# Performance work log

Measured on AMD Instinct MI355X. Metric: run time of the kernel, lower is better.

Reference implementation:

```python
import jax, jax.numpy as jnp
import numpy as np

B, S, D, H, NI, NB = 512, 200, 256, 4, 100000, 2
DH = D // H
NEG = float(-(2**32) + 1)
SCALE = float(1.0 / np.sqrt(DH))


def ln(x, g, b, eps=1e-3):
    # keras LayerNormalization (default epsilon=1e-3)
    m = jnp.mean(x, axis=-1, keepdims=True)
    v = jnp.var(x, axis=-1, keepdims=True)
    return (x - m) * jax.lax.rsqrt(v + eps) * g + b


def setup_inputs() -> dict:
    key = jax.random.key(0)
    ks = jax.random.split(key, 10)
    s = 0.02
    return {
        "input_ids": jax.random.randint(ks[0], (B, S), 0, NI + 1, dtype=jnp.int32),
        "item_emb": jax.random.normal(ks[1], (NI + 1, D), jnp.float32) * s,
        "pos_emb": jax.random.normal(ks[2], (S, D), jnp.float32) * s,
        "ln1_g": jnp.ones((NB, D), jnp.float32),
        "ln1_b": jnp.zeros((NB, D), jnp.float32),
        "wq": jax.random.normal(ks[3], (NB, D, D), jnp.float32) * s,
        "bq": jnp.zeros((NB, D), jnp.float32),
        "wk": jax.random.normal(ks[4], (NB, D, D), jnp.float32) * s,
        "bk": jnp.zeros((NB, D), jnp.float32),
        "wv": jax.random.normal(ks[5], (NB, D, D), jnp.float32) * s,
        "bv": jnp.zeros((NB, D), jnp.float32),
        "ln2_g": jnp.ones((NB, D), jnp.float32),
        "ln2_b": jnp.zeros((NB, D), jnp.float32),
        "wd": jax.random.normal(ks[6], (NB, D, D), jnp.float32) * s,
        "bd": jnp.zeros((NB, D), jnp.float32),
        "seq_g": jnp.ones((D,), jnp.float32),
        "seq_b": jnp.zeros((D,), jnp.float32),
        "out_item_emb": jax.random.normal(ks[7], (NI, D), jnp.float32) * s,
    }


def reference(input_ids, item_emb, pos_emb, ln1_g, ln1_b, wq, bq, wk, bk, wv, bv,
              ln2_g, ln2_b, wd, bd, seq_g, seq_b, out_item_emb):
    seq = item_emb[input_ids] + pos_emb[None]                      # [B,S,D]
    mask = (input_ids != NI).astype(seq.dtype)[:, :, None]        # pad id == num_items
    causal = jnp.tril(jnp.ones((S, S), bool))
    for i in range(NB):
        x = ln(seq, ln1_g[i], ln1_b[i])                            # queries (pre-norm)
        q = (x @ wq[i] + bq[i]).reshape(B, S, H, DH).transpose(0, 2, 1, 3)
        k = (seq @ wk[i] + bk[i]).reshape(B, S, H, DH).transpose(0, 2, 1, 3)
        v = (seq @ wv[i] + bv[i]).reshape(B, S, H, DH).transpose(0, 2, 1, 3)
        scores = jnp.einsum('bhqd,bhkd->bhqk', q, k) * SCALE       # [B,H,S,S]
        scores = jnp.where(causal, scores, NEG)
        attn = jax.nn.softmax(scores, axis=-1)
        o = jnp.einsum('bhqk,bhkd->bhqd', attn, v)
        o = o.transpose(0, 2, 1, 3).reshape(B, S, D)
        x2 = o + x                                                 # residual to normed queries
        y = jax.nn.relu(ln(x2, ln2_g[i], ln2_b[i]) @ wd[i] + bd[i])
        seq = (y + x2) * mask
    seq_emb = ln(seq[:, -1, :], seq_g, seq_b)                      # [B,D]
    return seq_emb @ out_item_emb.T                                # [B,num_items], linear act
```

## Files before the change

### kernel.cpp

```cpp
#include <hip/hip_runtime.h>
#include <hip/hip_bf16.h>
#include <cstdint>
#include <cstddef>

namespace {
constexpr int B = 512, S = 200, D = 256, H = 4, DH = 64, NI = 100000;
constexpr float EPS = 1e-3f;
constexpr float SCALE = 0.125f;
}

typedef __attribute__((ext_vector_type(8))) short bf16x8;
typedef __attribute__((ext_vector_type(4))) float f32x4;

__device__ inline unsigned short f2b(float f) {
  union { float f; unsigned int u; } v; v.f = f;
  unsigned int r = v.u + 0x7FFFu + ((v.u >> 16) & 1u);
  return (unsigned short)(r >> 16);
}

__device__ inline float b2f(unsigned short u) {
  union { unsigned int i; float f; } x; x.i = (unsigned int)u << 16; return x.f;
}

__device__ inline bf16x8 pack8(float4 a, float4 b) {
  bf16x8 r;
  r[0] = (short)f2b(a.x); r[1] = (short)f2b(a.y); r[2] = (short)f2b(a.z); r[3] = (short)f2b(a.w);
  r[4] = (short)f2b(b.x); r[5] = (short)f2b(b.y); r[6] = (short)f2b(b.z); r[7] = (short)f2b(b.w);
  return r;
}

__device__ inline ushort4 pack4(float4 a) {
  ushort4 r;
  r.x = f2b(a.x); r.y = f2b(a.y); r.z = f2b(a.z); r.w = f2b(a.w);
  return r;
}

__device__ inline float4 unpack4(ushort4 u) {
  float4 r; r.x = b2f(u.x); r.y = b2f(u.y); r.z = b2f(u.z); r.w = b2f(u.w); return r;
}

__device__ inline void gload_lds16(const unsigned short* g, unsigned short* l) {
  __builtin_amdgcn_global_load_lds((const __attribute__((address_space(1))) void*)g,
                                   (__attribute__((address_space(3))) void*)l, 16, 0, 0);
}

__global__ void cvt_wt_k(const float* __restrict__ wq, const float* __restrict__ wk,
                         const float* __restrict__ wv, const float* __restrict__ wd,
                         unsigned short* __restrict__ dst) {
  const int t = blockIdx.x * 256 + threadIdx.x;
  const int w = t >> 14, rem = t & 16383;
  const int k = rem >> 6, n4 = (rem & 63) * 4;
  const int blk = w >> 2, which = w & 3;
  const float* src = (which == 0 ? wq : which == 1 ? wk : which == 2 ? wv : wd) + blk * 65536;
  const float4 v = *(const float4*)(src + k * 256 + n4);
  unsigned short* d = dst + w * 65536;
  d[(n4 + 0) * 256 + k] = f2b(v.x);
  d[(n4 + 1) * 256 + k] = f2b(v.y);
  d[(n4 + 2) * 256 + k] = f2b(v.z);
  d[(n4 + 3) * 256 + k] = f2b(v.w);
}

__global__ __launch_bounds__(256) void embed_ln_k(const int* __restrict__ ids,
                                                  const float* __restrict__ ie,
                                                  const float* __restrict__ pe,
                                                  const float* __restrict__ g1,
                                                  const float* __restrict__ b1,
                                                  unsigned short* __restrict__ seq_bf,
                                                  unsigned short* __restrict__ x_bf) {
  const int row = blockIdx.x * 4 + (threadIdx.x >> 6);
  const int lane = threadIdx.x & 63;
  const int id = ids[row];
  const int s = row % S;
  float4 v = *(const float4*)(ie + (size_t)id * D + (lane << 2));
  const float4 p = *(const float4*)(pe + (size_t)s * D + (lane << 2));
  v.x += p.x; v.y += p.y; v.z += p.z; v.w += p.w;
  *(ushort4*)(seq_bf + (size_t)row * D + (lane << 2)) = pack4(v);
  const float4 vb = unpack4(pack4(v));
  float su = vb.x + vb.y + vb.z + vb.w;
  float ss = vb.x * vb.x + vb.y * vb.y + vb.z * vb.z + vb.w * vb.w;
#pragma unroll
  for (int off = 32; off; off >>= 1) {
    su += __shfl_xor(su, off);
    ss += __shfl_xor(ss, off);
  }
  const float mean = su * (1.f / D);
  const float rs = rsqrtf(ss * (1.f / D) - mean * mean + EPS);
  const float4 gv = *(const float4*)(g1 + (lane << 2));
  const float4 bv = *(const float4*)(b1 + (lane << 2));
  float4 o;
  o.x = (vb.x - mean) * rs * gv.x + bv.x;
  o.y = (vb.y - mean) * rs * gv.y + bv.y;
  o.z = (vb.z - mean) * rs * gv.z + bv.z;
  o.w = (vb.w - mean) * rs * gv.w + bv.w;
  *(ushort4*)(x_bf + (size_t)row * D + (lane << 2)) = pack4(o);
}

__global__ __launch_bounds__(256) void ln_bf_k(const unsigned short* __restrict__ in,
                                               size_t in_stride,
                                               const float* __restrict__ g, const float* __restrict__ b,
                                               unsigned short* __restrict__ outp, int nrows) {
  const int row = blockIdx.x * 4 + (threadIdx.x >> 6);
  if (row >= nrows) return;
  const int lane = threadIdx.x & 63;
  const float4 v = unpack4(*(const ushort4*)(in + (size_t)row * in_stride + (lane << 2)));
  float s = v.x + v.y + v.z + v.w;
  float ss = v.x * v.x + v.y * v.y + v.z * v.z + v.w * v.w;
#pragma unroll
  for (int off = 32; off; off >>= 1) {
    s += __shfl_xor(s, off);
    ss += __shfl_xor(ss, off);
  }
  const float mean = s * (1.f / D);
  const float rs = rsqrtf(ss * (1.f / D) - mean * mean + EPS);
  const float4 gv = *(const float4*)(g + (lane << 2));
  const float4 bv = *(const float4*)(b + (lane << 2));
  float4 o;
  o.x = (v.x - mean) * rs * gv.x + bv.x;
  o.y = (v.y - mean) * rs * gv.y + bv.y;
  o.z = (v.z - mean) * rs * gv.z + bv.z;
  o.w = (v.w - mean) * rs * gv.w + bv.w;
  *(ushort4*)(outp + (size_t)row * D + (lane << 2)) = pack4(o);
}

__global__ __launch_bounds__(512) void bgemm2_k(const unsigned short* __restrict__ A,
                                                const unsigned short* __restrict__ Wt,
                                                const float* __restrict__ bias,
                                                unsigned short* __restrict__ Cbf, float osc) {
  __shared__ unsigned short As[128 * 64];
  __shared__ unsigned short Bs[256 * 64];
  const int tid = threadIdx.x, w = tid >> 6, lane = tid & 63;
  const int kb = lane >> 4, ln = lane & 15;
  const int m0 = blockIdx.x * 128;
  const int wm = w & 1, wn = w >> 1;

  f32x4 acc[4][4];
#pragma unroll
  for (int i = 0; i < 4; ++i)
#pragma unroll
    for (int j = 0; j < 4; ++j) acc[i][j] = (f32x4){0.f, 0.f, 0.f, 0.f};

  for (int ks = 0; ks < 4; ++ks) {
    const int ko = ks * 64;
#pragma unroll
    for (int r = 0; r < 2; ++r) {
      const int g = (w * 2 + r) * 64 + lane;
      const int row = g >> 3, gc = g & 7;
      gload_lds16(A + (size_t)(m0 + row) * 256 + ko + ((gc ^ (row & 7)) << 3),
                  As + (size_t)(w * 2 + r) * 512);
    }
#pragma unroll
    for (int r = 0; r < 4; ++r) {
      const int g = (w * 4 + r) * 64 + lane;
      const int row = g >> 3, gc = g & 7;
      gload_lds16(Wt + (size_t)row * 256 + ko + ((gc ^ (row & 7)) << 3),
                  Bs + (size_t)(w * 4 + r) * 512);
    }
    __syncthreads();
#pragma unroll
    for (int h = 0; h < 2; ++h) {
      bf16x8 af[4], bfr[4];
#pragma unroll
      for (int i = 0; i < 4; ++i) {
        const int ar = wm * 64 + i * 16 + ln;
        af[i] = *(const bf16x8*)(As + ar * 64 + (((h * 64 + kb * 16) ^ ((ar & 7) << 4)) >> 1));
        const int br = wn * 64 + i * 16 + ln;
        bfr[i] = *(const bf16x8*)(Bs + br * 64 + (((h * 64 + kb * 16) ^ ((br & 7) << 4)) >> 1));
      }
#pragma unroll
      for (int i = 0; i < 4; ++i)
#pragma unroll
        for (int j = 0; j < 4; ++j)
          acc[i][j] = __builtin_amdgcn_mfma_f32_16x16x32_bf16(af[i], bfr[j], acc[i][j], 0, 0, 0);
    }
    __syncthreads();
  }

  const int crow0 = m0 + wm * 64 + kb * 4;
  const int ccol0 = wn * 64 + ln;
#pragma unroll
  for (int j = 0; j < 4; ++j) {
    const int col = ccol0 + j * 16;
    const float bj = bias[col];
#pragma unroll
    for (int i = 0; i < 4; ++i) {
#pragma unroll
      for (int r = 0; r < 4; ++r) {
        const int row = crow0 + i * 16 + r;
        Cbf[(size_t)row * 256 + col] = f2b((acc[i][j][r] + bj) * osc);
      }
    }
  }
}

template <int LN1>
__global__ __launch_bounds__(256) void ffn_k(const unsigned short* __restrict__ x_bf,
                                             const unsigned short* __restrict__ o_bf,
                                             const unsigned short* __restrict__ Wt,
                                             const float* __restrict__ bias,
                                             const float* __restrict__ g2,
                                             const float* __restrict__ b2,
                                             const int* __restrict__ ids,
                                             unsigned short* __restrict__ seq_out,
                                             const float* __restrict__ g1,
                                             const float* __restrict__ b1,
                                             unsigned short* __restrict__ x1) {
  __shared__ unsigned short Xt[64 * 256];
  __shared__ unsigned short Bs[256 * 64];
  __shared__ float stats[64][2];
  __shared__ float params[512];
  const int tid = threadIdx.x, w = tid >> 6, lane = tid & 63;
  const int kb = lane >> 4, ln = lane & 15;
  const int m0 = blockIdx.x * 64;
  const int wn = w;

  params[tid] = g2[tid & 255];
  params[256 + (tid & 255)] = b2[tid & 255];
#pragma unroll
  for (int it = 0; it < 8; ++it) {
    const int g = it * 256 + tid;
    const int row = g >> 5, gc = g & 31;
    const bf16x8 xv = *(const bf16x8*)(x_bf + (size_t)(m0 + row) * 256 + gc * 8);
    const bf16x8 ov = *(const bf16x8*)(o_bf + (size_t)(m0 + row) * 256 + gc * 8);
    bf16x8 sv;
#pragma unroll
    for (int e = 0; e < 8; ++e)
      sv[e] = (short)f2b(b2f((unsigned short)xv[e]) + b2f((unsigned short)ov[e]));
    *(bf16x8*)(Xt + row * 256 + (((gc * 16) ^ ((row & 7) << 4)) >> 1)) = sv;
  }
  __syncthreads();
  {
    const int srow = tid >> 2, sq = tid & 3;
    float su = 0.f, ssq = 0.f;
#pragma unroll
    for (int gg = 0; gg < 8; ++gg) {
      const int gc = sq * 8 + gg;
      const bf16x8 v = *(const bf16x8*)(Xt + srow * 256 + (((gc * 16) ^ ((srow & 7) << 4)) >> 1));
#pragma unroll
      for (int e = 0; e < 8; ++e) {
        const float f = b2f((unsigned short)v[e]);
        su += f; ssq += f * f;
      }
    }
    su += __shfl_xor(su, 1); ssq += __shfl_xor(ssq, 1);
    su += __shfl_xor(su, 2); ssq += __shfl_xor(ssq, 2);
    if (sq == 0) {
      const float mean = su * (1.f / D);
      stats[srow][0] = mean;
      stats[srow][1] = rsqrtf(ssq * (1.f / D) - mean * mean + EPS);
    }
  }
  __syncthreads();
  float ep[4][4][4];
  const int ccl = wn * 64 + ln;
#pragma unroll
  for (int i = 0; i < 4; ++i)
#pragma unroll
    for (int j = 0; j < 4; ++j)
#pragma unroll
      for (int r = 0; r < 4; ++r) {
        const int rr = i * 16 + kb * 4 + r;
        const int col = ccl + j * 16;
        ep[i][j][r] = b2f(Xt[rr * 256 + (((col * 2) ^ ((rr & 7) << 4)) >> 1)]);
      }
  __syncthreads();
#pragma unroll
  for (int it = 0; it < 8; ++it) {
    const int g = it * 256 + tid;
    const int row = g >> 5, gc = g & 31;
    const int idx = row * 256 + (((gc * 16) ^ ((row & 7) << 4)) >> 1);
    const bf16x8 v = *(const bf16x8*)(Xt + idx);
    const float mu = stats[row][0], rs = stats[row][1];
    bf16x8 t;
#pragma unroll
    for (int e = 0; e < 8; ++e) {
      const int k = gc * 8 + e;
      t[e] = (short)f2b((b2f((unsigned short)v[e]) - mu) * rs * params[k] + params[256 + k]);
    }
    *(bf16x8*)(Xt + idx) = t;
  }
  __syncthreads();
  f32x4 acc[4][4];
#pragma unroll
  for (int i = 0; i < 4; ++i)
#pragma unroll
    for (int j = 0; j < 4; ++j) acc[i][j] = (f32x4){0.f, 0.f, 0.f, 0.f};

  for (int ks = 0; ks < 4; ++ks) {
#pragma unroll
    for (int r = 0; r < 8; ++r) {
      const int g = (w * 8 + r) * 64 + lane;
      const int row = g >> 3, gc = g & 7;
      gload_lds16(Wt + (size_t)row * 256 + ks * 64 + ((gc ^ (row & 7)) << 3),
                  Bs + (size_t)(w * 8 + r) * 512);
    }
    __syncthreads();
#pragma unroll
    for (int h = 0; h < 2; ++h) {
      bf16x8 af[4], bfr[4];
#pragma unroll
      for (int i = 0; i < 4; ++i) {
        const int ar = i * 16 + ln;
        af[i] = *(const bf16x8*)(Xt + ar * 256 +
                                 ((ks * 128 + ((h * 64 + kb * 16) ^ ((ar & 7) << 4))) >> 1));
        const int br = wn * 64 + i * 16 + ln;
        bfr[i] = *(const bf16x8*)(Bs + br * 64 + (((h * 64 + kb * 16) ^ ((br & 7) << 4)) >> 1));
      }
#pragma unroll
      for (int i = 0; i < 4; ++i)
#pragma unroll
        for (int j = 0; j < 4; ++j)
          acc[i][j] = __builtin_amdgcn_mfma_f32_16x16x32_bf16(af[i], bfr[j], acc[i][j], 0, 0, 0);
    }
    __syncthreads();
  }
  float mk[4][4];
#pragma unroll
  for (int i = 0; i < 4; ++i)
#pragma unroll
    for (int r = 0; r < 4; ++r)
      mk[i][r] = (ids[m0 + i * 16 + kb * 4 + r] != NI) ? 1.f : 0.f;
#pragma unroll
  for (int j = 0; j < 4; ++j) {
    const int col = ccl + j * 16;
    const float bj = bias[col];
#pragma unroll
    for (int i = 0; i < 4; ++i) {
#pragma unroll
      for (int r = 0; r < 4; ++r) {
        const int grow = m0 + i * 16 + kb * 4 + r;
        float v = fmaxf(acc[i][j][r] + bj, 0.f);
        v = (v + ep[i][j][r]) * mk[i][r];
        const unsigned short vb = f2b(v);
        seq_out[(size_t)grow * 256 + col] = vb;
        if (LN1) acc[i][j][r] = b2f(vb);
      }
    }
  }
  if (LN1) {
    float s_[4][4], ss_[4][4];
#pragma unroll
    for (int i = 0; i < 4; ++i)
#pragma unroll
      for (int r = 0; r < 4; ++r) {
        float s = 0.f, ss = 0.f;
#pragma unroll
        for (int j = 0; j < 4; ++j) { const float v = acc[i][j][r]; s += v; ss += v * v; }
#pragma unroll
        for (int off = 1; off < 16; off <<= 1) {
          s += __shfl_xor(s, off);
          ss += __shfl_xor(ss, off);
        }
        s_[i][r] = s; ss_[i][r] = ss;
      }
    float* red = params;
    __syncthreads();
    if (ln == 0) {
#pragma unroll
      for (int i = 0; i < 4; ++i)
#pragma unroll
        for (int r = 0; r < 4; ++r) {
          const int rt = i * 16 + kb * 4 + r;
          red[rt * 8 + wn * 2 + 0] = s_[i][r];
          red[rt * 8 + wn * 2 + 1] = ss_[i][r];
        }
    }
    __syncthreads();
#pragma unroll
    for (int i = 0; i < 4; ++i)
#pragma unroll
      for (int r = 0; r < 4; ++r) {
        const int rt = i * 16 + kb * 4 + r;
        float Sv = 0.f, SS = 0.f;
#pragma unroll
        for (int q = 0; q < 4; ++q) { Sv += red[rt * 8 + q * 2]; SS += red[rt * 8 + q * 2 + 1]; }
        const float mean = Sv * (1.f / D);
        s_[i][r] = mean;
        ss_[i][r] = rsqrtf(SS * (1.f / D) - mean * mean + EPS);
      }
#pragma unroll
    for (int j = 0; j < 4; ++j) {
      const int col = ccl + j * 16;
      const float gc = g1[col], bc = b1[col];
#pragma unroll
      for (int i = 0; i < 4; ++i) {
#pragma unroll
        for (int r = 0; r < 4; ++r) {
          const int grow = m0 + i * 16 + kb * 4 + r;
          const float xv = (acc[i][j][r] - s_[i][r]) * ss_[i][r] * gc + bc;
          x1[(size_t)grow * 256 + col] = f2b(xv);
        }
      }
    }
  }
}

__global__ __launch_bounds__(256) void logits_k(const unsigned short* __restrict__ A,
                                                const float* __restrict__ Wf,
                                                float* __restrict__ C) {
  __shared__ unsigned short Bs[128 * 256];
  __shared__ unsigned short As[128 * 256];
  const int tid = threadIdx.x, w = tid >> 6, lane = tid & 63;
  const int kb = lane >> 4, ln = lane & 15;
  const int wm = w & 1, wn = w >> 1;
  const int n0 = blockIdx.x * 128;
#pragma unroll
  for (int it = 0; it < 16; ++it) {
    const int g = it * 256 + tid;
    const int row = g >> 5, gc = g & 31;
    int br = n0 + row; if (br > NI - 1) br = NI - 1;
    const float* src = Wf + (size_t)br * 256 + gc * 8;
    const float4 f0 = *(const float4*)src;
    const float4 f1 = *(const float4*)(src + 4);
    *(bf16x8*)(Bs + row * 256 + (((gc * 16) ^ ((row & 7) << 4)) >> 1)) = pack8(f0, f1);
  }
  for (int m = 0; m < 4; ++m) {
    const int m0 = m * 128;
#pragma unroll
    for (int it = 0; it < 16; ++it) {
      const int g = it * 256 + w * 64 + lane;
      const int row = g >> 5, gc = g & 31;
      gload_lds16(A + (size_t)(m0 + row) * 256 + (((gc * 16) ^ ((row & 7) << 4)) >> 1),
                  As + (size_t)(it * 256 + w * 64) * 8);
    }
    __syncthreads();
    f32x4 acc[4][4];
#pragma unroll
    for (int i = 0; i < 4; ++i)
#pragma unroll
      for (int j = 0; j < 4; ++j) acc[i][j] = (f32x4){0.f, 0.f, 0.f, 0.f};
#pragma unroll
    for (int ks = 0; ks < 4; ++ks) {
#pragma unroll
      for (int h = 0; h < 2; ++h) {
        bf16x8 af[4], bfr[4];
#pragma unroll
        for (int i = 0; i < 4; ++i) {
          const int ar = wm * 64 + i * 16 + ln;
          af[i] = *(const bf16x8*)(As + ar * 256 +
                                   ((ks * 128 + ((h * 64 + kb * 16) ^ ((ar & 7) << 4))) >> 1));
          const int br = wn * 64 + i * 16 + ln;
          bfr[i] = *(const bf16x8*)(Bs + br * 256 +
                                    ((ks * 128 + ((h * 64 + kb * 16) ^ ((br & 7) << 4))) >> 1));
        }
#pragma unroll
        for (int i = 0; i < 4; ++i)
#pragma unroll
          for (int j = 0; j < 4; ++j)
            acc[i][j] = __builtin_amdgcn_mfma_f32_16x16x32_bf16(af[i], bfr[j], acc[i][j], 0, 0, 0);
      }
    }
    const int crow0 = m0 + wm * 64 + kb * 4;
    const int ccol0 = n0 + wn * 64 + ln;
#pragma unroll
    for (int j = 0; j < 4; ++j) {
      const int col = ccol0 + j * 16;
      if (col >= NI) continue;
#pragma unroll
      for (int i = 0; i < 4; ++i) {
#pragma unroll
        for (int r = 0; r < 4; ++r) {
          const int row = crow0 + i * 16 + r;
          C[(size_t)row * NI + col] = acc[i][j][r];
        }
      }
    }
    __syncthreads();
  }
}

__global__ __launch_bounds__(256) void attn_k(const unsigned short* __restrict__ Q,
                                              const unsigned short* __restrict__ Kg,
                                              const unsigned short* __restrict__ Vg,
                                              unsigned short* __restrict__ O) {
  __shared__ unsigned short Ks[13312];
  __shared__ unsigned short Vt[13312];
  __shared__ unsigned short Ps[4 * 3328];
  const int b = blockIdx.x >> 2;
  const int h = blockIdx.x & 3;
  const int tid = threadIdx.x, w = tid >> 6, lane = tid & 63;
  const int kb = lane >> 4, ln = lane & 15;
  const size_t base = (size_t)b * S * D + h * DH;

  for (int s = w; s < 26; s += 4) {
    const int t = s >> 1, h2 = s & 1;
    int krow = t * 16 + ln; if (krow > S - 1) krow = S - 1;
    gload_lds16(Kg + base + (size_t)krow * D + h2 * 32 + kb * 8, Ks + s * 512);
  }
  for (int g = tid; g < 200 * 8; g += 256) {
    const int key = g >> 3, d0 = (g & 7) * 8;
    const bf16x8 v = *(const bf16x8*)(Vg + base + (size_t)key * D + d0);
#pragma unroll
    for (int i = 0; i < 8; ++i) {
      const int d = d0 + i, ct = d >> 4, cl = d & 15;
      int addr;
      if (key < 192) addr = (((ct * 6 + (key >> 5)) * 4 + ((key >> 3) & 3)) * 16 + cl) * 8 + (key & 7);
      else           addr = 12288 + ((ct * 2 + ((key >> 3) & 1)) * 16 + cl) * 8 + (key & 7);
      Vt[addr] = (unsigned short)v[i];
    }
  }
  if (tid < 64) {
    const int ct = tid >> 4, cl = tid & 15;
    *(bf16x8*)(Vt + 12288 + ((ct * 2 + 1) * 16 + cl) * 8) = (bf16x8)0;
  }
  __syncthreads();
  unsigned short* Pw = Ps + w * 3328;

#pragma unroll
  for (int it = 0; it < 4; ++it) {
    const int c = (it == 0) ? (12 - w) : (it == 1) ? (5 + w) : (it == 2) ? (4 - w)
                                                                         : (w == 3 ? 0 : -1);
    if (c < 0) continue;
    const int q0 = c << 4;
    const int tmax = (c | 1) > 12 ? 12 : (c | 1);
    const int ktm = c >> 1;

    int qr = q0 + ln; if (qr > S - 1) qr = S - 1;
    const unsigned short* qp = Q + base + (size_t)qr * D + kb * 8;
    const bf16x8 aq0 = *(const bf16x8*)(qp);
    const bf16x8 aq1 = *(const bf16x8*)(qp + 32);
    f32x4 sc[13];
#pragma unroll
    for (int t = 0; t < 13; ++t) {
      if (t <= tmax) {
        f32x4 a = {0.f, 0.f, 0.f, 0.f};
        a = __builtin_amdgcn_mfma_f32_16x16x32_bf16(aq0, *(const bf16x8*)(Ks + (t * 2 + 0) * 512 + lane * 8), a, 0, 0, 0);
        a = __builtin_amdgcn_mfma_f32_16x16x32_bf16(aq1, *(const bf16x8*)(Ks + (t * 2 + 1) * 512 + lane * 8), a, 0, 0, 0);
        sc[t] = a;
      }
    }
    float inv[4];
#pragma unroll
    for (int r = 0; r < 4; ++r) {
      const int q = q0 + kb * 4 + r;
      const int qrow = kb * 4 + r;
      float m = -1e30f;
#pragma unroll
      for (int t = 0; t < 13; ++t) {
        if (t <= tmax) {
          const int j = t * 16 + ln;
          float s = sc[t][r];
          s = (j <= q) ? s : -1e30f;
          sc[t][r] = s;
          m = fmaxf(m, s);
        }
      }
      m = fmaxf(m, __shfl_xor(m, 1));
      m = fmaxf(m, __shfl_xor(m, 2));
      m = fmaxf(m, __shfl_xor(m, 4));
      m = fmaxf(m, __shfl_xor(m, 8));
      float sm = 0.f;
#pragma unroll
      for (int t = 0; t < 13; ++t) {
        if (t <= tmax) {
          const float e = __expf(sc[t][r] - m);
          sm += e;
          int addr;
          if (t < 12) addr = (((t >> 1) * 4 + ((2 * t + (ln >> 3)) & 3)) * 16 + qrow) * 8 + (ln & 7);
          else        addr = 3072 + ((ln >> 3) * 16 + qrow) * 8 + (ln & 7);
          Pw[addr] = f2b(e);
        }
      }
      sm += __shfl_xor(sm, 1);
      sm += __shfl_xor(sm, 2);
      sm += __shfl_xor(sm, 4);
      sm += __shfl_xor(sm, 8);
      inv[r] = 1.f / sm;
    }
#pragma unroll
    for (int ct = 0; ct < 4; ++ct) {
      f32x4 a = {0.f, 0.f, 0.f, 0.f};
#pragma unroll
      for (int kt = 0; kt < 6; ++kt) {
        if (kt <= ktm) {
          const bf16x8 pa = *(const bf16x8*)(Pw + ((kt * 4 + kb) * 16 + ln) * 8);
          const bf16x8 vb = *(const bf16x8*)(Vt + (((ct * 6 + kt) * 4 + kb) * 16 + ln) * 8);
          a = __builtin_amdgcn_mfma_f32_16x16x32_bf16(pa, vb, a, 0, 0, 0);
        }
      }
      if (c == 12) {
        bf16x8 pa = (bf16x8)0, vb = (bf16x8)0;
        if (kb < 2) {
          pa = *(const bf16x8*)(Pw + 3072 + (kb * 16 + ln) * 8);
          vb = *(const bf16x8*)(Vt + 12288 + ((ct * 2 + kb) * 16 + ln) * 8);
        }
        a = __builtin_amdgcn_mfma_f32_16x16x32_bf16(pa, vb, a, 0, 0, 0);
      }
#pragma unroll
      for (int r = 0; r < 4; ++r) {
        const int q = q0 + kb * 4 + r;
        if (q < S) O[base + (size_t)q * D + ct * 16 + ln] = f2b(a[r] * inv[r]);
      }
    }
  }
}

extern "C" void kernel_launch(void* const* d_in, const int* in_sizes, int n_in,
                              void* d_out, int out_size, void* d_ws, size_t ws_size,
                              hipStream_t stream) {
  const int* ids        = (const int*)d_in[0];
  const float* item_emb = (const float*)d_in[1];
  const float* pos_emb  = (const float*)d_in[2];
  const float* ln1_g    = (const float*)d_in[3];
  const float* ln1_b    = (const float*)d_in[4];
  const float* wq       = (const float*)d_in[5];
  const float* bq       = (const float*)d_in[6];
  const float* wk       = (const float*)d_in[7];
  const float* bk       = (const float*)d_in[8];
  const float* wv       = (const float*)d_in[9];
  const float* bv       = (const float*)d_in[10];
  const float* ln2_g    = (const float*)d_in[11];
  const float* ln2_b    = (const float*)d_in[12];
  const float* wd       = (const float*)d_in[13];
  const float* bd       = (const float*)d_in[14];
  const float* seq_g    = (const float*)d_in[15];
  const float* seq_b    = (const float*)d_in[16];
  const float* w_out    = (const float*)d_in[17];
  float* out = (float*)d_out;

  char* wsb = (char*)d_ws;
  unsigned short* seq_bf = (unsigned short*)(wsb + 0);
  unsigned short* x_bf   = (unsigned short*)(wsb + 52428800);
  unsigned short* q_bf   = (unsigned short*)(wsb + 104857600);
  unsigned short* k_bf   = (unsigned short*)(wsb + 157286400);
  unsigned short* v_bf   = (unsigned short*)(wsb + 209715200);
  unsigned short* o_bf   = (unsigned short*)(wsb + 262144000);
  unsigned short* wtb    = (unsigned short*)(wsb + 314572800);
  unsigned short* semb   = (unsigned short*)(wsb + 315621376);

  const int M = B * S;
  const int ln_grid = (M + 3) / 4;

  cvt_wt_k<<<512, 256, 0, stream>>>(wq, wk, wv, wd, wtb);
  embed_ln_k<<<ln_grid, 256, 0, stream>>>(ids, item_emb, pos_emb, ln1_g, ln1_b, seq_bf, x_bf);

  for (int blk = 0; blk < 2; ++blk) {
    const unsigned short* WT = wtb + (size_t)blk * 4 * 65536;

    bgemm2_k<<<800, 512, 0, stream>>>(seq_bf, WT + 1 * 65536, bk + blk * D, k_bf, 1.f);
    bgemm2_k<<<800, 512, 0, stream>>>(seq_bf, WT + 2 * 65536, bv + blk * D, v_bf, 1.f);
    bgemm2_k<<<800, 512, 0, stream>>>(x_bf, WT + 0 * 65536, bq + blk * D, q_bf, SCALE);
    attn_k<<<B * H, 256, 0, stream>>>(q_bf, k_bf, v_bf, o_bf);
    if (blk == 0) {
      ffn_k<1><<<1600, 256, 0, stream>>>(x_bf, o_bf, WT + 3 * 65536, bd + blk * D,
                                         ln2_g + blk * D, ln2_b + blk * D, ids, seq_bf,
                                         ln1_g + D, ln1_b + D, x_bf);
    } else {
      ffn_k<0><<<1600, 256, 0, stream>>>(x_bf, o_bf, WT + 3 * 65536, bd + blk * D,
                                         ln2_g + blk * D, ln2_b + blk * D, ids, seq_bf,
                                         nullptr, nullptr, nullptr);
    }
  }

  ln_bf_k<<<(B + 3) / 4, 256, 0, stream>>>(seq_bf + (size_t)(S - 1) * D, (size_t)S * D,
                                           seq_g, seq_b, semb, B);
  logits_k<<<782, 256, 0, stream>>>(semb, w_out, out);
}
```

Before: 737.5 us.

## Fuse K/V projections sharing one LDS A tile; read weights directly from global

Replaces the per-projection 128x256 GEMM kernel with a 64-row kernel that loads the whole 64x256 activation tile into LDS once. For K and V it reuses that tile for both weight matrices in one launch, so seq is read once instead of twice. Weight fragments in both the projection kernel and the FFN kernel are now read straight from global memory (expected to hit cache) rather than staged through LDS, which removes the per-k-step syncs and cuts LDS use. The cost is uncoalesced-ish per-lane global weight reads in the inner loop, which depend on L1/L2 hit rates.

```diff
diff --git a/kernel.cpp b/kernel.cpp
--- a/kernel.cpp
+++ b/kernel.cpp
@@ -122,71 +122,74 @@
   *(ushort4*)(outp + (size_t)row * D + (lane << 2)) = pack4(o);
 }
 
-__global__ __launch_bounds__(512) void bgemm2_k(const unsigned short* __restrict__ A,
-                                                const unsigned short* __restrict__ Wt,
-                                                const float* __restrict__ bias,
-                                                unsigned short* __restrict__ Cbf, float osc) {
-  __shared__ unsigned short As[128 * 64];
-  __shared__ unsigned short Bs[256 * 64];
+template <int TWO>
+__global__ __launch_bounds__(256) void qkv_k(const unsigned short* __restrict__ A,
+                                             const unsigned short* __restrict__ Wt0,
+                                             const float* __restrict__ b0,
+                                             unsigned short* __restrict__ C0,
+                                             const unsigned short* __restrict__ Wt1,
+                                             const float* __restrict__ b1,
+                                             unsigned short* __restrict__ C1, float osc) {
+  __shared__ unsigned short As[64 * 256];
   const int tid = threadIdx.x, w = tid >> 6, lane = tid & 63;
   const int kb = lane >> 4, ln = lane & 15;
-  const int m0 = blockIdx.x * 128;
-  const int wm = w & 1, wn = w >> 1;
-
-  f32x4 acc[4][4];
-#pragma unroll
-  for (int i = 0; i < 4; ++i)
-#pragma unroll
-    for (int j = 0; j < 4; ++j) acc[i][j] = (f32x4){0.f, 0.f, 0.f, 0.f};
-
-  for (int ks = 0; ks < 4; ++ks) {
-    const int ko = ks * 64;
-#pragma unroll
-    for (int r = 0; r < 2; ++r) {
-      const int g = (w * 2 + r) * 64 + lane;
-      const int row = g >> 3, gc = g & 7;
-      gload_lds16(A + (size_t)(m0 + row) * 256 + ko + ((gc ^ (row & 7)) << 3),
-                  As + (size_t)(w * 2 + r) * 512);
-    }
-#pragma unroll
-    for (int r = 0; r < 4; ++r) {
-      const int g = (w * 4 + r) * 64 + lane;
-      const int row = g >> 3, gc = g & 7;
-      gload_lds16(Wt + (size_t)row * 256 + ko + ((gc ^ (row & 7)) << 3),
-                  Bs + (size_t)(w * 4 + r) * 512);
-    }
-    __syncthreads();
-#pragma unroll
-    for (int h = 0; h < 2; ++h) {
-      bf16x8 af[4], bfr[4];
+  const int m0 = blockIdx.x * 64;
+  const int wn = w;
+
+#pragma unroll
+  for (int it = 0; it < 8; ++it) {
+    const int g = it * 256 + tid;
+    const int row = g >> 5, gc = g & 31;
+    gload_lds16(A + (size_t)(m0 + row) * 256 + (gc ^ (row & 7)) * 8,
+                As + (size_t)(it * 256 + w * 64) * 8);
+  }
+  __syncthreads();
+
+#pragma unroll
+  for (int which = 0; which < 1 + TWO; ++which) {
+    const unsigned short* Wt = which ? Wt1 : Wt0;
+    const float* bias = which ? b1 : b0;
+    unsigned short* C = which ? C1 : C0;
+    const float sc = which ? 1.f : osc;
+
+    f32x4 acc[4][4];
+#pragma unroll
+    for (int i = 0; i < 4; ++i)
+#pragma unroll
+      for (int j = 0; j < 4; ++j) acc[i][j] = (f32x4){0.f, 0.f, 0.f, 0.f};
+
+#pragma unroll
+    for (int ks = 0; ks < 4; ++ks) {
+#pragma unroll
+      for (int h = 0; h < 2; ++h) {
+        bf16x8 af[4], bfr[4];
+#pragma unroll
+        for (int i = 0; i < 4; ++i) {
+          const int ar = i * 16 + ln;
+          af[i] = *(const bf16x8*)(As + ar * 256 +
+                                   ((ks * 128 + ((h * 64 + kb * 16) ^ ((ar & 7) << 4))) >> 1));
+          bfr[i] = *(const bf16x8*)(Wt + (size_t)(wn * 64 + i * 16 + ln) * 256 +
+                                    ks * 64 + h * 32 + kb * 8);
+        }
+#pragma unroll
+        for (int i = 0; i < 4; ++i)
+#pragma unroll
+          for (int j = 0; j < 4; ++j)
+            acc[i][j] = __builtin_amdgcn_mfma_f32_16x16x32_bf16(af[i], bfr[j], acc[i][j], 0, 0, 0);
+      }
+    }
+    const int ccl = wn * 64 + ln;
+#pragma unroll
+    for (int j = 0; j < 4; ++j) {
+      const int col = ccl + j * 16;
+      const float bj = bias[col];
 #pragma unroll
       for (int i = 0; i < 4; ++i) {
-        const int ar = wm * 64 + i * 16 + ln;
-        af[i] = *(const bf16x8*)(As + ar * 64 + (((h * 64 + kb * 16) ^ ((ar & 7) << 4)) >> 1));
-        const int br = wn * 64 + i * 16 + ln;
-        bfr[i] = *(const bf16x8*)(Bs + br * 64 + (((h * 64 + kb * 16) ^ ((br & 7) << 4)) >> 1));
-      }
-#pragma unroll
-      for (int i = 0; i < 4; ++i)
-#pragma unroll
-        for (int j = 0; j < 4; ++j)
-          acc[i][j] = __builtin_amdgcn_mfma_f32_16x16x32_bf16(af[i], bfr[j], acc[i][j], 0, 0, 0);
-    }
-    __syncthreads();
-  }
-
-  const int crow0 = m0 + wm * 64 + kb * 4;
-  const int ccol0 = wn * 64 + ln;
-#pragma unroll
-  for (int j = 0; j < 4; ++j) {
-    const int col = ccol0 + j * 16;
-    const float bj = bias[col];
-#pragma unroll
-    for (int i = 0; i < 4; ++i) {
-#pragma unroll
-      for (int r = 0; r < 4; ++r) {
-        const int row = crow0 + i * 16 + r;
-        Cbf[(size_t)row * 256 + col] = f2b((acc[i][j][r] + bj) * osc);
+#pragma unroll
+        for (int r = 0; r < 4; ++r) {
+          const int row = m0 + i * 16 + kb * 4 + r;
+          C[(size_t)row * 256 + col] = f2b((acc[i][j][r] + bj) * sc);
+        }
       }
     }
   }
@@ -205,7 +208,6 @@
                                              const float* __restrict__ b1,
                                              unsigned short* __restrict__ x1) {
   __shared__ unsigned short Xt[64 * 256];
-  __shared__ unsigned short Bs[256 * 64];
   __shared__ float stats[64][2];
   __shared__ float params[512];
   const int tid = threadIdx.x, w = tid >> 6, lane = tid & 63;
@@ -285,15 +287,8 @@
 #pragma unroll
     for (int j = 0; j < 4; ++j) acc[i][j] = (f32x4){0.f, 0.f, 0.f, 0.f};
 
+#pragma unroll
   for (int ks = 0; ks < 4; ++ks) {
-#pragma unroll
-    for (int r = 0; r < 8; ++r) {
-      const int g = (w * 8 + r) * 64 + lane;
-      const int row = g >> 3, gc = g & 7;
-      gload_lds16(Wt + (size_t)row * 256 + ks * 64 + ((gc ^ (row & 7)) << 3),
-                  Bs + (size_t)(w * 8 + r) * 512);
-    }
-    __syncthreads();
 #pragma unroll
     for (int h = 0; h < 2; ++h) {
       bf16x8 af[4], bfr[4];
@@ -302,8 +297,8 @@
         const int ar = i * 16 + ln;
         af[i] = *(const bf16x8*)(Xt + ar * 256 +
                                  ((ks * 128 + ((h * 64 + kb * 16) ^ ((ar & 7) << 4))) >> 1));
-        const int br = wn * 64 + i * 16 + ln;
-        bfr[i] = *(const bf16x8*)(Bs + br * 64 + (((h * 64 + kb * 16) ^ ((br & 7) << 4)) >> 1));
+        bfr[i] = *(const bf16x8*)(Wt + (size_t)(wn * 64 + i * 16 + ln) * 256 +
+                                  ks * 64 + h * 32 + kb * 8);
       }
 #pragma unroll
       for (int i = 0; i < 4; ++i)
@@ -311,7 +306,6 @@
         for (int j = 0; j < 4; ++j)
           acc[i][j] = __builtin_amdgcn_mfma_f32_16x16x32_bf16(af[i], bfr[j], acc[i][j], 0, 0, 0);
     }
-    __syncthreads();
   }
   float mk[4][4];
 #pragma unroll
@@ -636,9 +630,10 @@
   for (int blk = 0; blk < 2; ++blk) {
     const unsigned short* WT = wtb + (size_t)blk * 4 * 65536;
 
-    bgemm2_k<<<800, 512, 0, stream>>>(seq_bf, WT + 1 * 65536, bk + blk * D, k_bf, 1.f);
-    bgemm2_k<<<800, 512, 0, stream>>>(seq_bf, WT + 2 * 65536, bv + blk * D, v_bf, 1.f);
-    bgemm2_k<<<800, 512, 0, stream>>>(x_bf, WT + 0 * 65536, bq + blk * D, q_bf, SCALE);
+    qkv_k<1><<<1600, 256, 0, stream>>>(seq_bf, WT + 1 * 65536, bk + blk * D, k_bf,
+                                       WT + 2 * 65536, bv + blk * D, v_bf, 1.f);
+    qkv_k<0><<<1600, 256, 0, stream>>>(x_bf, WT + 0 * 65536, bq + blk * D, q_bf,
+                                       nullptr, nullptr, nullptr, SCALE);
     attn_k<<<B * H, 256, 0, stream>>>(q_bf, k_bf, v_bf, o_bf);
     if (blk == 0) {
       ffn_k<1><<<1600, 256, 0, stream>>>(x_bf, o_bf, WT + 3 * 65536, bd + blk * D,
```

New measurement: 766.8 us. 1.04x slower.
